# Kernel optimization log

Measured on AMD Instinct MI355X. Metric: run time of the kernel, lower is better.

## Reference

```python
import jax, jax.numpy as jnp
import numpy as np

EPS_BN = 1e-5


def _batchnorm(h, g, b):
    # training-mode BatchNorm1d over the flattened (B*N*k) axis
    mu = jnp.mean(h, axis=0)
    var = jnp.var(h, axis=0)
    return g * (h - mu) * jax.lax.rsqrt(var + EPS_BN) + b


def setup_inputs() -> dict:
    key = jax.random.key(0)
    ks = jax.random.split(key, 5)
    B, N = 4, 8192
    x = jax.random.normal(ks[0], (B, N, 3), dtype=jnp.float32)
    W1 = jax.random.normal(ks[1], (7, 10), dtype=jnp.float32) * (1.0 / np.sqrt(7.0))
    b1 = jax.random.normal(ks[2], (10,), dtype=jnp.float32) * 0.01
    W2 = jax.random.normal(ks[3], (10, 10), dtype=jnp.float32) * (1.0 / np.sqrt(10.0))
    b2 = jax.random.normal(ks[4], (10,), dtype=jnp.float32) * 0.01
    g1 = jnp.ones((10,), jnp.float32); be1 = jnp.zeros((10,), jnp.float32)
    g2 = jnp.ones((10,), jnp.float32); be2 = jnp.zeros((10,), jnp.float32)
    return {"x": x, "W1": W1, "b1": b1, "g1": g1, "be1": be1,
            "W2": W2, "b2": b2, "g2": g2, "be2": be2, "k": 9}


def reference(x, W1, b1, g1, be1, W2, b2, g2, be2, k):
    B, N, C = x.shape
    # --- kNN graph (brute force, self included as nearest) ---
    sq = jnp.sum(x * x, axis=-1)                                    # (B,N)
    d2 = sq[:, :, None] + sq[:, None, :] - 2.0 * jnp.einsum('bnc,bmc->bnm', x, x)
    _, idx = jax.lax.top_k(-d2, k + 1)                              # (B,N,k+1)
    nbrs = x[jnp.arange(B)[:, None, None], idx]                     # (B,N,k+1,3)
    rel = (nbrs - x[:, :, None, :])[:, :, 1:, :]                    # drop self -> (B,N,k,3)
    # --- sort neighbors by azimuth phi = atan2(y, x) ---
    phi = jnp.arctan2(rel[..., 1], rel[..., 0])                     # (B,N,k)
    order = jnp.argsort(phi, axis=-1)
    v1 = jnp.take_along_axis(rel, order[..., None], axis=2)         # (B,N,k,3)
    v2 = jnp.roll(v1, -1, axis=2)                                   # next neighbor (cyclic)
    # --- umbrella-style surface features ---
    centroids = 0.5 * (v1 + v2)
    normals = jnp.cross(v1, v2)
    normals = normals / (jnp.linalg.norm(normals, axis=-1, keepdims=True) + 1e-6)
    sign = jnp.where(normals[..., 0:1, 0] > 0, 1.0, -1.0)[..., None]  # (B,N,1,1)
    normals = normals * sign
    position = jnp.sum(normals * centroids, axis=-1, keepdims=True) / jnp.sqrt(jnp.asarray(3.0, x.dtype))
    feat = jnp.concatenate([centroids, normals, position], axis=-1)   # (B,N,k,7)
    feat = feat.reshape(B * N * k, 7)
    # --- tiny MLP + max-pool over k ---
    h = jax.nn.relu(_batchnorm(feat @ W1 + b1, g1, be1))
    h = jax.nn.relu(_batchnorm(h @ W2 + b2, g2, be2))
    return jnp.max(h.reshape(B, N, k, 10), axis=2)                  # (B,N,10)
```

## Files before the change

kernel.cpp:

```cpp
#include <hip/hip_runtime.h>
#include <math.h>
#include <float.h>
#include <stdint.h>

#define B_ 4
#define N_ 8192
#define K_ 9
#define NPTS (B_ * N_)
#define NROWS (NPTS * K_)
#define SPLIT 8
#define CHUNK (N_ / SPLIT)
#define NGROUP 32
#define GSIZE (CHUNK / NGROUP)
#define GSTRIDE 33
#define NCOPY 16

typedef float f4 __attribute__((ext_vector_type(4)));
typedef float f32x2 __attribute__((ext_vector_type(2)));

__device__ __forceinline__ f32x2 dist2_pk(f32x2 xx, f32x2 yy, f32x2 zz, f32x2 ww,
                                          f32x2 qx, f32x2 qy, f32x2 qz, f32x2 qw) {
  f32x2 t0 = qx * xx;
  f32x2 t1 = __builtin_elementwise_fma(qy, yy, t0);
  f32x2 t2 = __builtin_elementwise_fma(qz, zz, t1);
  f32x2 s  = qw + ww;
  f32x2 m2 = {-2.0f, -2.0f};
  return __builtin_elementwise_fma(t2, m2, s);
}

#define GDECL(G) float gd##G; int gi##G;
#define SCANG(G)                                                           \
  { float bgd = FLT_MAX; int bq = 0;                                       \
    _Pragma("clang loop unroll(disable)")                                  \
    for (int pr = 0; pr < 16; pr += 4) {                                   \
      const f4* cp = CH + (G * GSTRIDE + 2 * pr);                          \
      f4 A0 = cp[0], B0 = cp[1], A1 = cp[2], B1 = cp[3];                   \
      f4 A2 = cp[4], B2 = cp[5], A3 = cp[6], B3 = cp[7];                   \
      f32x2 dA = dist2_pk(__builtin_shufflevector(A0, A0, 0, 1),           \
                          __builtin_shufflevector(A0, A0, 2, 3),           \
                          __builtin_shufflevector(B0, B0, 0, 1),           \
                          __builtin_shufflevector(B0, B0, 2, 3),           \
                          qx2, qy2, qz2, qw2);                             \
      f32x2 dB = dist2_pk(__builtin_shufflevector(A1, A1, 0, 1),           \
                          __builtin_shufflevector(A1, A1, 2, 3),           \
                          __builtin_shufflevector(B1, B1, 0, 1),           \
                          __builtin_shufflevector(B1, B1, 2, 3),           \
                          qx2, qy2, qz2, qw2);                             \
      f32x2 dC = dist2_pk(__builtin_shufflevector(A2, A2, 0, 1),           \
                          __builtin_shufflevector(A2, A2, 2, 3),           \
                          __builtin_shufflevector(B2, B2, 0, 1),           \
                          __builtin_shufflevector(B2, B2, 2, 3),           \
                          qx2, qy2, qz2, qw2);                             \
      f32x2 dD = dist2_pk(__builtin_shufflevector(A3, A3, 0, 1),           \
                          __builtin_shufflevector(A3, A3, 2, 3),           \
                          __builtin_shufflevector(B3, B3, 0, 1),           \
                          __builtin_shufflevector(B3, B3, 2, 3),           \
                          qx2, qy2, qz2, qw2);                             \
      float d0 = dA.x, d1 = dA.y, d2 = dB.x, d3 = dB.y;                    \
      float d4 = dC.x, d5 = dC.y, d6 = dD.x, d7 = dD.y;                    \
      if (HS) {                                                            \
        int j = G * GSIZE + 2 * pr;                                        \
        d0 = (j + 0 == nl) ? FLT_MAX : d0;                                 \
        d1 = (j + 1 == nl) ? FLT_MAX : d1;                                 \
        d2 = (j + 2 == nl) ? FLT_MAX : d2;                                 \
        d3 = (j + 3 == nl) ? FLT_MAX : d3;                                 \
        d4 = (j + 4 == nl) ? FLT_MAX : d4;                                 \
        d5 = (j + 5 == nl) ? FLT_MAX : d5;                                 \
        d6 = (j + 6 == nl) ? FLT_MAX : d6;                                 \
        d7 = (j + 7 == nl) ? FLT_MAX : d7;                                 \
      }                                                                    \
      float m = fminf(fminf(fminf(d0, d1), fminf(d2, d3)),                 \
                      fminf(fminf(d4, d5), fminf(d6, d7)));                \
      bool lt = m < bgd; bgd = lt ? m : bgd; bq = lt ? pr : bq;            \
    }                                                                      \
    gd##G = bgd; gi##G = -1 - bq; }
#define LMC(G, S)                                                          \
  { bool lt = gd##G < wd##S;                                               \
    wd##S = lt ? gd##G : wd##S; wi##S = lt ? gi##G : wi##S;                \
    wg##S = lt ? G : wg##S; }
#define CMB(S)                                                             \
  { bool lt = wd##S < wda;                                                 \
    wda = lt ? wd##S : wda; wia = lt ? wi##S : wia; wga = lt ? wg##S : wga; }
#define WBK(G)                                                             \
  { bool m = (wg == G); gd##G = m ? nd : gd##G; gi##G = m ? ni : gi##G; }
#define TOURN8()                                                           \
  float e01d, e23d, e45d, e67d, f03d, f47d, md;                            \
  int   e01i, e23i, e45i, e67i, f03i, f47i, mi;                            \
  { bool t;                                                                \
    t = d1 < d0; e01d = t ? d1 : d0; e01i = t ? (j + 1) : (j + 0);         \
    t = d3 < d2; e23d = t ? d3 : d2; e23i = t ? (j + 3) : (j + 2);         \
    t = d5 < d4; e45d = t ? d5 : d4; e45i = t ? (j + 5) : (j + 4);         \
    t = d7 < d6; e67d = t ? d7 : d6; e67i = t ? (j + 7) : (j + 6);         \
    t = e23d < e01d; f03d = t ? e23d : e01d; f03i = t ? e23i : e01i;       \
    t = e67d < e45d; f47d = t ? e67d : e45d; f47i = t ? e67i : e45i;       \
    t = f47d < f03d; md = t ? f47d : f03d; mi = t ? f47i : f03i; }

template <bool HS>
__device__ __forceinline__ void knn_chunk(const f4* CH, f32x2 qx2, f32x2 qy2,
                                          f32x2 qz2, f32x2 qw2,
                                          int nl, int j0, int s, int p,
                                          uint2* __restrict__ PBDI) {
  GDECL(0) GDECL(1) GDECL(2) GDECL(3) GDECL(4) GDECL(5) GDECL(6) GDECL(7)
  GDECL(8) GDECL(9) GDECL(10) GDECL(11) GDECL(12) GDECL(13) GDECL(14) GDECL(15)
  GDECL(16) GDECL(17) GDECL(18) GDECL(19) GDECL(20) GDECL(21) GDECL(22) GDECL(23)
  GDECL(24) GDECL(25) GDECL(26) GDECL(27) GDECL(28) GDECL(29) GDECL(30) GDECL(31)

  SCANG(0) SCANG(1) SCANG(2) SCANG(3) SCANG(4) SCANG(5) SCANG(6) SCANG(7)
  SCANG(8) SCANG(9) SCANG(10) SCANG(11) SCANG(12) SCANG(13) SCANG(14) SCANG(15)
  SCANG(16) SCANG(17) SCANG(18) SCANG(19) SCANG(20) SCANG(21) SCANG(22) SCANG(23)
  SCANG(24) SCANG(25) SCANG(26) SCANG(27) SCANG(28) SCANG(29) SCANG(30) SCANG(31)

#pragma clang loop unroll(disable)
  for (int r = 0; r < K_; ++r) {
    float wda = gd0; int wia = gi0; int wga = 0;
    LMC(1,a) LMC(2,a) LMC(3,a) LMC(4,a) LMC(5,a) LMC(6,a) LMC(7,a)
    float wdb = gd8; int wib = gi8; int wgb = 8;
    LMC(9,b) LMC(10,b) LMC(11,b) LMC(12,b) LMC(13,b) LMC(14,b) LMC(15,b)
    float wdc = gd16; int wic = gi16; int wgc = 16;
    LMC(17,c) LMC(18,c) LMC(19,c) LMC(20,c) LMC(21,c) LMC(22,c) LMC(23,c)
    float wdd = gd24; int wid = gi24; int wgd = 24;
    LMC(25,d) LMC(26,d) LMC(27,d) LMC(28,d) LMC(29,d) LMC(30,d) LMC(31,d)
    CMB(b) CMB(c) CMB(d)
    float wd = wda; int wist = wia; int wg = wga;

    int ab = wg * GSTRIDE;
    int jb = wg * GSIZE;

    int wi;
    {
      int bq = (wist >= 0) ? 0 : (-1 - wist);
      const f4* cp = CH + (ab + 2 * bq);
      f4 A0 = cp[0], B0 = cp[1], A1 = cp[2], B1 = cp[3];
      f4 A2 = cp[4], B2 = cp[5], A3 = cp[6], B3 = cp[7];
      int j = jb + 2 * bq;
      f32x2 dA = dist2_pk(__builtin_shufflevector(A0, A0, 0, 1),
                          __builtin_shufflevector(A0, A0, 2, 3),
                          __builtin_shufflevector(B0, B0, 0, 1),
                          __builtin_shufflevector(B0, B0, 2, 3),
                          qx2, qy2, qz2, qw2);
      f32x2 dB = dist2_pk(__builtin_shufflevector(A1, A1, 0, 1),
                          __builtin_shufflevector(A1, A1, 2, 3),
                          __builtin_shufflevector(B1, B1, 0, 1),
                          __builtin_shufflevector(B1, B1, 2, 3),
                          qx2, qy2, qz2, qw2);
      f32x2 dC = dist2_pk(__builtin_shufflevector(A2, A2, 0, 1),
                          __builtin_shufflevector(A2, A2, 2, 3),
                          __builtin_shufflevector(B2, B2, 0, 1),
                          __builtin_shufflevector(B2, B2, 2, 3),
                          qx2, qy2, qz2, qw2);
      f32x2 dD = dist2_pk(__builtin_shufflevector(A3, A3, 0, 1),
                          __builtin_shufflevector(A3, A3, 2, 3),
                          __builtin_shufflevector(B3, B3, 0, 1),
                          __builtin_shufflevector(B3, B3, 2, 3),
                          qx2, qy2, qz2, qw2);
      float d0 = dA.x, d1 = dA.y, d2 = dB.x, d3 = dB.y;
      float d4 = dC.x, d5 = dC.y, d6 = dD.x, d7 = dD.y;
      if (HS) {
        d0 = (j + 0 == nl) ? FLT_MAX : d0;
        d1 = (j + 1 == nl) ? FLT_MAX : d1;
        d2 = (j + 2 == nl) ? FLT_MAX : d2;
        d3 = (j + 3 == nl) ? FLT_MAX : d3;
        d4 = (j + 4 == nl) ? FLT_MAX : d4;
        d5 = (j + 5 == nl) ? FLT_MAX : d5;
        d6 = (j + 6 == nl) ? FLT_MAX : d6;
        d7 = (j + 7 == nl) ? FLT_MAX : d7;
      }
      const int IMX = 0x7fffffff;
      int a0 = (d0 == wd) ? (j + 0) : IMX;
      int a1 = (d1 == wd) ? (j + 1) : IMX;
      int a2 = (d2 == wd) ? (j + 2) : IMX;
      int a3 = (d3 == wd) ? (j + 3) : IMX;
      int a4 = (d4 == wd) ? (j + 4) : IMX;
      int a5 = (d5 == wd) ? (j + 5) : IMX;
      int a6 = (d6 == wd) ? (j + 6) : IMX;
      int a7 = (d7 == wd) ? (j + 7) : IMX;
      int m01 = a0 < a1 ? a0 : a1;
      int m23 = a2 < a3 ? a2 : a3;
      int m45 = a4 < a5 ? a4 : a5;
      int m67 = a6 < a7 ? a6 : a7;
      int mA = m01 < m23 ? m01 : m23;
      int mB = m45 < m67 ? m45 : m67;
      int jm = mA < mB ? mA : mB;
      wi = (wist >= 0) ? wist : jm;
    }

    uint2 o; o.x = __float_as_uint(wd); o.y = (unsigned)(j0 + wi);
    PBDI[(size_t)(s * K_ + r) * NPTS + p] = o;

    float nd = FLT_MAX; int ni = 0;
#pragma clang loop unroll(disable)
    for (int pr = 0; pr < 16; pr += 4) {
      const f4* cp = CH + (ab + 2 * pr);
      f4 A0 = cp[0], B0 = cp[1], A1 = cp[2], B1 = cp[3];
      f4 A2 = cp[4], B2 = cp[5], A3 = cp[6], B3 = cp[7];
      int j = jb + 2 * pr;
      f32x2 dA = dist2_pk(__builtin_shufflevector(A0, A0, 0, 1),
                          __builtin_shufflevector(A0, A0, 2, 3),
                          __builtin_shufflevector(B0, B0, 0, 1),
                          __builtin_shufflevector(B0, B0, 2, 3),
                          qx2, qy2, qz2, qw2);
      f32x2 dB = dist2_pk(__builtin_shufflevector(A1, A1, 0, 1),
                          __builtin_shufflevector(A1, A1, 2, 3),
                          __builtin_shufflevector(B1, B1, 0, 1),
                          __builtin_shufflevector(B1, B1, 2, 3),
                          qx2, qy2, qz2, qw2);
      f32x2 dC = dist2_pk(__builtin_shufflevector(A2, A2, 0, 1),
                          __builtin_shufflevector(A2, A2, 2, 3),
                          __builtin_shufflevector(B2, B2, 0, 1),
                          __builtin_shufflevector(B2, B2, 2, 3),
                          qx2, qy2, qz2, qw2);
      f32x2 dD = dist2_pk(__builtin_shufflevector(A3, A3, 0, 1),
                          __builtin_shufflevector(A3, A3, 2, 3),
                          __builtin_shufflevector(B3, B3, 0, 1),
                          __builtin_shufflevector(B3, B3, 2, 3),
                          qx2, qy2, qz2, qw2);
      float d0 = dA.x, d1 = dA.y, d2 = dB.x, d3 = dB.y;
      float d4 = dC.x, d5 = dC.y, d6 = dD.x, d7 = dD.y;
      if (HS) {
        d0 = (j + 0 == nl) ? FLT_MAX : d0;
        d1 = (j + 1 == nl) ? FLT_MAX : d1;
        d2 = (j + 2 == nl) ? FLT_MAX : d2;
        d3 = (j + 3 == nl) ? FLT_MAX : d3;
        d4 = (j + 4 == nl) ? FLT_MAX : d4;
        d5 = (j + 5 == nl) ? FLT_MAX : d5;
        d6 = (j + 6 == nl) ? FLT_MAX : d6;
        d7 = (j + 7 == nl) ? FLT_MAX : d7;
      }
      bool k0 = (d0 > wd) | ((d0 == wd) & ((j + 0) > wi));
      bool k1 = (d1 > wd) | ((d1 == wd) & ((j + 1) > wi));
      bool k2 = (d2 > wd) | ((d2 == wd) & ((j + 2) > wi));
      bool k3 = (d3 > wd) | ((d3 == wd) & ((j + 3) > wi));
      bool k4 = (d4 > wd) | ((d4 == wd) & ((j + 4) > wi));
      bool k5 = (d5 > wd) | ((d5 == wd) & ((j + 5) > wi));
      bool k6 = (d6 > wd) | ((d6 == wd) & ((j + 6) > wi));
      bool k7 = (d7 > wd) | ((d7 == wd) & ((j + 7) > wi));
      d0 = k0 ? d0 : FLT_MAX;
      d1 = k1 ? d1 : FLT_MAX;
      d2 = k2 ? d2 : FLT_MAX;
      d3 = k3 ? d3 : FLT_MAX;
      d4 = k4 ? d4 : FLT_MAX;
      d5 = k5 ? d5 : FLT_MAX;
      d6 = k6 ? d6 : FLT_MAX;
      d7 = k7 ? d7 : FLT_MAX;
      TOURN8();
      bool lt = md < nd; nd = lt ? md : nd; ni = lt ? mi : ni;
    }
    WBK(0) WBK(1) WBK(2) WBK(3) WBK(4) WBK(5) WBK(6) WBK(7)
    WBK(8) WBK(9) WBK(10) WBK(11) WBK(12) WBK(13) WBK(14) WBK(15)
    WBK(16) WBK(17) WBK(18) WBK(19) WBK(20) WBK(21) WBK(22) WBK(23)
    WBK(24) WBK(25) WBK(26) WBK(27) WBK(28) WBK(29) WBK(30) WBK(31)
  }
}

__launch_bounds__(128, 4)
__global__ void k_knn(const float* __restrict__ x, uint2* __restrict__ PBDI,
                      double* __restrict__ ACC) {
  __shared__ f4 CH[NGROUP * GSTRIDE];
  int bid = blockIdx.x;
  if (bid == 0) {
    for (int t = threadIdx.x; t < NCOPY * 40; t += 128) ACC[t] = 0.0;
  }
  int pg = bid >> 3;
  int s = bid & (SPLIT - 1);
  int p = pg * 128 + threadIdx.x;
  int b = p >> 13;
  int n = p & (N_ - 1);
  int bO = b * N_;
  int j0 = s * CHUNK;

  const float* xq = x + 3 * (size_t)p;
  float qa = xq[0], qb = xq[1], qc = xq[2];
  float qw = qa * qa + qb * qb + qc * qc;
  f32x2 qx2 = {qa, qa}, qy2 = {qb, qb}, qz2 = {qc, qc}, qw2 = {qw, qw};

  for (int u = threadIdx.x; u < CHUNK / 2; u += 128) {
    const float* xp = x + 3 * (size_t)(bO + j0 + 2 * u);
    float a0 = xp[0], b0 = xp[1], c0 = xp[2];
    float a1 = xp[3], b1 = xp[4], c1 = xp[5];
    int G = u >> 4, rr = u & 15;
    f4 lo = {a0, a1, b0, b1};
    f4 hi = {c0, c1, a0 * a0 + b0 * b0 + c0 * c0, a1 * a1 + b1 * b1 + c1 * c1};
    CH[G * GSTRIDE + 2 * rr] = lo;
    CH[G * GSTRIDE + 2 * rr + 1] = hi;
  }
  __syncthreads();

  int n0 = (pg * 128) & (N_ - 1);
  int nl = n - j0;
  if (s == (n0 >> 10)) knn_chunk<true >(CH, qx2, qy2, qz2, qw2, nl, j0, s, p, PBDI);
  else                 knn_chunk<false>(CH, qx2, qy2, qz2, qw2, nl, j0, s, p, PBDI);
}

#define LVL(bdv, biv)                                                     \
  { bool lt = cd < (bdv); float td = (bdv); int ti = (biv);               \
    (bdv) = lt ? cd : (bdv); (biv) = lt ? ci : (biv);                     \
    cd = lt ? td : cd; ci = lt ? ti : ci; }
#define INS9ALL()                                                         \
  LVL(b0d, b0i) LVL(b1d, b1i) LVL(b2d, b2i) LVL(b3d, b3i) LVL(b4d, b4i)  \
  LVL(b5d, b5i) LVL(b6d, b6i) LVL(b7d, b7i) LVL(b8d, b8i)
#define TOP9_DECL()                                                       \
  float b0d = FLT_MAX, b1d = FLT_MAX, b2d = FLT_MAX, b3d = FLT_MAX,       \
        b4d = FLT_MAX, b5d = FLT_MAX, b6d = FLT_MAX, b7d = FLT_MAX,       \
        b8d = FLT_MAX;                                                    \
  int b0i = 0, b1i = 0, b2i = 0, b3i = 0, b4i = 0, b5i = 0, b6i = 0,      \
      b7i = 0, b8i = 0;

#define MKREL(T)                                                          \
  float rx##T, ry##T, rz##T, ph##T;                                       \
  { const float* mp = x + 3 * (size_t)(bO + b##T##i);                     \
    rx##T = mp[0] - qa; ry##T = mp[1] - qb; rz##T = mp[2] - qc;           \
    ph##T = atan2f(ry##T, rx##T); }

#define CE(A, Bv)                                                         \
  { bool lt = ph##Bv < ph##A; float t0;                                   \
    t0 = ph##A; ph##A = lt ? ph##Bv : t0; ph##Bv = lt ? t0 : ph##Bv;      \
    t0 = rx##A; rx##A = lt ? rx##Bv : t0; rx##Bv = lt ? t0 : rx##Bv;      \
    t0 = ry##A; ry##A = lt ? ry##Bv : t0; ry##Bv = lt ? t0 : ry##Bv;      \
    t0 = rz##A; rz##A = lt ? rz##Bv : t0; rz##Bv = lt ? t0 : rz##Bv; }

#define ST9(arr, v0, v1, v2, v3, v4, v5, v6, v7, v8)                      \
  arr[0 * 64 + pl] = v0; arr[1 * 64 + pl] = v1; arr[2 * 64 + pl] = v2;    \
  arr[3 * 64 + pl] = v3; arr[4 * 64 + pl] = v4; arr[5 * 64 + pl] = v5;    \
  arr[6 * 64 + pl] = v6; arr[7 * 64 + pl] = v7; arr[8 * 64 + pl] = v8;

__launch_bounds__(256, 4)
__global__ void k_tail1(const float* __restrict__ x, const uint2* __restrict__ PBDI,
                        const float* __restrict__ W1, const float* __restrict__ b1,
                        float* __restrict__ H1, double* __restrict__ ACC) {
  __shared__ float  LMD[64 * 37];
  __shared__ int    LMI[64 * 37];
  __shared__ float  LREL[3][9 * 64];
  __shared__ float  LSGN[64];
  __shared__ double sred[4][20];

  int q = threadIdx.x >> 6;
  int pl = threadIdx.x & 63;
  int pbase = blockIdx.x * 64;
  int p = pbase + pl;

  {
    TOP9_DECL();
#pragma clang loop unroll_count(2)
    for (int e = 0; e < 2 * K_; ++e) {
      uint2 v = PBDI[(size_t)(q * 2 * K_ + e) * NPTS + p];
      float cd = __uint_as_float(v.x);
      int ci = (int)v.y;
      INS9ALL();
    }
    int base = pl * 37 + q * 9;
    LMD[base + 0] = b0d; LMD[base + 1] = b1d; LMD[base + 2] = b2d;
    LMD[base + 3] = b3d; LMD[base + 4] = b4d; LMD[base + 5] = b5d;
    LMD[base + 6] = b6d; LMD[base + 7] = b7d; LMD[base + 8] = b8d;
    LMI[base + 0] = b0i; LMI[base + 1] = b1i; LMI[base + 2] = b2i;
    LMI[base + 3] = b3i; LMI[base + 4] = b4i; LMI[base + 5] = b5i;
    LMI[base + 6] = b6i; LMI[base + 7] = b7i; LMI[base + 8] = b8i;
  }
  __syncthreads();

  if (q == 0) {
    int b = p >> 13;
    int bO = b * N_;
    const float* xq = x + 3 * (size_t)p;
    float qa = xq[0], qb = xq[1], qc = xq[2];

    TOP9_DECL();
#pragma clang loop unroll_count(3)
    for (int e = 0; e < 4 * K_; ++e) {
      float cd = LMD[pl * 37 + e];
      int ci = LMI[pl * 37 + e];
      INS9ALL();
    }

    MKREL(0) MKREL(1) MKREL(2) MKREL(3) MKREL(4)
    MKREL(5) MKREL(6) MKREL(7) MKREL(8)

    CE(0,1)
    CE(1,2) CE(0,1)
    CE(2,3) CE(1,2) CE(0,1)
    CE(3,4) CE(2,3) CE(1,2) CE(0,1)
    CE(4,5) CE(3,4) CE(2,3) CE(1,2) CE(0,1)
    CE(5,6) CE(4,5) CE(3,4) CE(2,3) CE(1,2) CE(0,1)
    CE(6,7) CE(5,6) CE(4,5) CE(3,4) CE(2,3) CE(1,2) CE(0,1)
    CE(7,8) CE(6,7) CE(5,6) CE(4,5) CE(3,4) CE(2,3) CE(1,2) CE(0,1)

    float nx0 = ry0 * rz1 - rz0 * ry1;
    float ny0 = rz0 * rx1 - rx0 * rz1;
    float nz0 = rx0 * ry1 - ry0 * rx1;
    float nrm0 = sqrtf(nx0 * nx0 + ny0 * ny0 + nz0 * nz0) + 1e-6f;
    LSGN[pl] = ((nx0 / nrm0) > 0.0f) ? 1.0f : -1.0f;

    ST9(LREL[0], rx0, rx1, rx2, rx3, rx4, rx5, rx6, rx7, rx8)
    ST9(LREL[1], ry0, ry1, ry2, ry3, ry4, ry5, ry6, ry7, ry8)
    ST9(LREL[2], rz0, rz1, rz2, rz3, rz4, rz5, rz6, rz7, rz8)
  }
  __syncthreads();

  double sum[10], ss[10];
#pragma unroll
  for (int c = 0; c < 10; ++c) { sum[c] = 0.0; ss[c] = 0.0; }

#pragma clang loop unroll(disable)
  for (int rl = threadIdx.x; rl < 9 * 64; rl += 256) {
    int t = rl >> 6;
    int pp = rl & 63;
    int t2 = (t + 1 == K_) ? 0 : t + 1;
    float v1x = LREL[0][t * 64 + pp];
    float v1y = LREL[1][t * 64 + pp];
    float v1z = LREL[2][t * 64 + pp];
    float v2x = LREL[0][t2 * 64 + pp];
    float v2y = LREL[1][t2 * 64 + pp];
    float v2z = LREL[2][t2 * 64 + pp];
    float sgn = LSGN[pp];

    float cx = 0.5f * (v1x + v2x);
    float cy = 0.5f * (v1y + v2y);
    float cz = 0.5f * (v1z + v2z);
    float nx = v1y * v2z - v1z * v2y;
    float ny = v1z * v2x - v1x * v2z;
    float nz = v1x * v2y - v1y * v2x;
    float nrm = sqrtf(nx * nx + ny * ny + nz * nz) + 1e-6f;
    nx /= nrm; ny /= nrm; nz /= nrm;
    nx *= sgn; ny *= sgn; nz *= sgn;
    float pos = (nx * cx + ny * cy + nz * cz) / 1.7320508075688772f;

    float fv[7] = {cx, cy, cz, nx, ny, nz, pos};
#pragma unroll
    for (int c = 0; c < 10; ++c) {
      float h = b1[c];
#pragma unroll
      for (int rr = 0; rr < 7; ++rr) h = fmaf(fv[rr], W1[rr * 10 + c], h);
      H1[(size_t)c * NROWS + (size_t)t * NPTS + pbase + pp] = h;
      double hd = (double)h;
      sum[c] += hd; ss[c] += hd * hd;
    }
  }

  int lane = threadIdx.x & 63, wv = threadIdx.x >> 6;
#pragma unroll
  for (int c = 0; c < 10; ++c) {
    double a = sum[c];
#pragma unroll
    for (int off = 32; off > 0; off >>= 1) a += __shfl_down(a, off);
    if (lane == 0) sred[wv][c] = a;
    double qq = ss[c];
#pragma unroll
    for (int off = 32; off > 0; off >>= 1) qq += __shfl_down(qq, off);
    if (lane == 0) sred[wv][10 + c] = qq;
  }
  __syncthreads();
  if (threadIdx.x < 20) {
    atomicAdd(&ACC[(blockIdx.x & (NCOPY - 1)) * 40 + threadIdx.x],
              sred[0][threadIdx.x] + sred[1][threadIdx.x] +
              sred[2][threadIdx.x] + sred[3][threadIdx.x]);
  }
}

__launch_bounds__(64)
__global__ void k_mlp2(const float* __restrict__ H1, double* __restrict__ ACC,
                       const float* __restrict__ g1, const float* __restrict__ be1,
                       const float* __restrict__ W2, const float* __restrict__ b2,
                       const float* __restrict__ g2, float* __restrict__ EXT) {
  __shared__ float MR[20];
  __shared__ double sred[20];
  if (threadIdx.x < 20) {
    int c = threadIdx.x % 10;
    int half = threadIdx.x / 10;
    double s0 = 0.0, s1 = 0.0;
#pragma unroll
    for (int cc = 0; cc < NCOPY; ++cc) {
      s0 += ACC[cc * 40 + c];
      s1 += ACC[cc * 40 + 10 + c];
    }
    double mu = s0 / (double)NROWS;
    double var = s1 / (double)NROWS - mu * mu;
    MR[threadIdx.x] = half ? (float)(1.0 / sqrt(var + 1e-5)) : (float)mu;
  }
  __syncthreads();

  int p = blockIdx.x * 64 + threadIdx.x;
  double sum[10], ss[10];
  float ext[10], sg[10];
#pragma unroll
  for (int c = 0; c < 10; ++c) {
    sum[c] = 0.0; ss[c] = 0.0;
    sg[c] = g2[c];
    ext[c] = (sg[c] >= 0.0f) ? -FLT_MAX : FLT_MAX;
  }

#pragma clang loop unroll(disable)
  for (int t = 0; t < K_; ++t) {
    float v[10];
#pragma unroll
    for (int c = 0; c < 10; ++c) {
      float h = H1[(size_t)c * NROWS + (size_t)t * NPTS + p];
      float z = g1[c] * (h - MR[c]) * MR[10 + c] + be1[c];
      v[c] = z > 0.0f ? z : 0.0f;
    }
#pragma unroll
    for (int c = 0; c < 10; ++c) {
      float h = b2[c];
#pragma unroll
      for (int u = 0; u < 10; ++u) h = fmaf(v[u], W2[u * 10 + c], h);
      sum[c] += (double)h;
      ss[c] += (double)h * (double)h;
      ext[c] = (sg[c] >= 0.0f) ? fmaxf(ext[c], h) : fminf(ext[c], h);
    }
  }

#pragma unroll
  for (int c = 0; c < 10; ++c)
    EXT[(size_t)c * NPTS + p] = ext[c];

#pragma unroll
  for (int c = 0; c < 10; ++c) {
    double a = sum[c];
#pragma unroll
    for (int off = 32; off > 0; off >>= 1) a += __shfl_down(a, off);
    if (threadIdx.x == 0) sred[c] = a;
    double qq = ss[c];
#pragma unroll
    for (int off = 32; off > 0; off >>= 1) qq += __shfl_down(qq, off);
    if (threadIdx.x == 0) sred[10 + c] = qq;
  }
  __syncthreads();
  if (threadIdx.x < 20) {
    atomicAdd(&ACC[(blockIdx.x & (NCOPY - 1)) * 40 + 20 + threadIdx.x],
              sred[threadIdx.x]);
  }
}

__launch_bounds__(64)
__global__ void k_out(const float* __restrict__ EXT, const double* __restrict__ ACC,
                      const float* __restrict__ g2, const float* __restrict__ be2,
                      float* __restrict__ out) {
  __shared__ float MR[20];
  if (threadIdx.x < 20) {
    int c = threadIdx.x % 10;
    int half = threadIdx.x / 10;
    double s0 = 0.0, s1 = 0.0;
#pragma unroll
    for (int cc = 0; cc < NCOPY; ++cc) {
      s0 += ACC[cc * 40 + 20 + c];
      s1 += ACC[cc * 40 + 30 + c];
    }
    double mu = s0 / (double)NROWS;
    double var = s1 / (double)NROWS - mu * mu;
    MR[threadIdx.x] = half ? (float)(1.0 / sqrt(var + 1e-5)) : (float)mu;
  }
  __syncthreads();

  int p = blockIdx.x * 64 + threadIdx.x;
#pragma unroll
  for (int c = 0; c < 10; ++c) {
    float h = EXT[(size_t)c * NPTS + p];
    float z = g2[c] * (h - MR[c]) * MR[10 + c] + be2[c];
    z = z > 0.0f ? z : 0.0f;
    out[(size_t)p * 10 + c] = z;
  }
}

extern "C" void kernel_launch(void* const* d_in, const int* in_sizes, int n_in,
                              void* d_out, int out_size, void* d_ws, size_t ws_size,
                              hipStream_t stream) {
  (void)in_sizes; (void)n_in; (void)out_size; (void)ws_size;
  const float* x  = (const float*)d_in[0];
  const float* W1 = (const float*)d_in[1];
  const float* b1 = (const float*)d_in[2];
  const float* g1 = (const float*)d_in[3];
  const float* be1= (const float*)d_in[4];
  const float* W2 = (const float*)d_in[5];
  const float* b2 = (const float*)d_in[6];
  const float* g2 = (const float*)d_in[7];
  const float* be2= (const float*)d_in[8];
  float* out = (float*)d_out;

  char* base = (char*)d_ws;
  uint2*  PBDI = (uint2*)base;
  float*  H1 = (float*)(base + (size_t)SPLIT * K_ * NPTS * 8);
  double* ACC = (double*)(H1 + (size_t)10 * NROWS);
  float*  EXT = (float*)PBDI;

  k_knn<<<(NPTS / 128) * SPLIT, 128, 0, stream>>>(x, PBDI, ACC);
  k_tail1<<<NPTS / 64, 256, 0, stream>>>(x, PBDI, W1, b1, H1, ACC);
  k_mlp2<<<NPTS / 64, 64, 0, stream>>>(H1, ACC, g1, be1, W2, b2, g2, EXT);
  k_out<<<NPTS / 64, 64, 0, stream>>>(EXT, ACC, g2, be2, out);
}
```

Before: 215.7 us.

## Parallelize k_mlp2 across neighbors with one wave per k slot

k_mlp2 previously looped over the 9 neighbors serially within a 64-thread block. Now each block has 576 threads, one wavefront per neighbor slot. Each wave computes the second-layer outputs in parallel, stores them in LDS, and then reduces max/min over k from shared memory. The intent is more parallelism and latency hiding for this small kernel. The cost is more LDS use, a block-wide barrier, and more shuffle reductions per row.

```diff
diff --git a/kernel.cpp b/kernel.cpp
--- a/kernel.cpp
+++ b/kernel.cpp
@@ -455,16 +455,18 @@
   }
 }
 
-__launch_bounds__(64)
+__launch_bounds__(576)
 __global__ void k_mlp2(const float* __restrict__ H1, double* __restrict__ ACC,
                        const float* __restrict__ g1, const float* __restrict__ be1,
                        const float* __restrict__ W2, const float* __restrict__ b2,
                        const float* __restrict__ g2, float* __restrict__ EXT) {
   __shared__ float MR[20];
-  __shared__ double sred[20];
-  if (threadIdx.x < 20) {
-    int c = threadIdx.x % 10;
-    int half = threadIdx.x / 10;
+  __shared__ float H2L[10][K_][64];
+  __shared__ double sred[9][20];
+  int tid = threadIdx.x;
+  if (tid < 20) {
+    int c = tid % 10;
+    int half = tid / 10;
     double s0 = 0.0, s1 = 0.0;
 #pragma unroll
     for (int cc = 0; cc < NCOPY; ++cc) {
@@ -473,59 +475,66 @@
     }
     double mu = s0 / (double)NROWS;
     double var = s1 / (double)NROWS - mu * mu;
-    MR[threadIdx.x] = half ? (float)(1.0 / sqrt(var + 1e-5)) : (float)mu;
-  }
-  __syncthreads();
-
-  int p = blockIdx.x * 64 + threadIdx.x;
-  double sum[10], ss[10];
-  float ext[10], sg[10];
+    MR[tid] = half ? (float)(1.0 / sqrt(var + 1e-5)) : (float)mu;
+  }
+  __syncthreads();
+
+  int t = tid >> 6;
+  int pl = tid & 63;
+  int pbase = blockIdx.x * 64;
+  int p = pbase + pl;
+
+  float v[10];
 #pragma unroll
   for (int c = 0; c < 10; ++c) {
-    sum[c] = 0.0; ss[c] = 0.0;
-    sg[c] = g2[c];
-    ext[c] = (sg[c] >= 0.0f) ? -FLT_MAX : FLT_MAX;
-  }
-
-#pragma clang loop unroll(disable)
-  for (int t = 0; t < K_; ++t) {
-    float v[10];
-#pragma unroll
-    for (int c = 0; c < 10; ++c) {
-      float h = H1[(size_t)c * NROWS + (size_t)t * NPTS + p];
-      float z = g1[c] * (h - MR[c]) * MR[10 + c] + be1[c];
-      v[c] = z > 0.0f ? z : 0.0f;
-    }
-#pragma unroll
-    for (int c = 0; c < 10; ++c) {
-      float h = b2[c];
-#pragma unroll
-      for (int u = 0; u < 10; ++u) h = fmaf(v[u], W2[u * 10 + c], h);
-      sum[c] += (double)h;
-      ss[c] += (double)h * (double)h;
-      ext[c] = (sg[c] >= 0.0f) ? fmaxf(ext[c], h) : fminf(ext[c], h);
-    }
-  }
-
-#pragma unroll
-  for (int c = 0; c < 10; ++c)
-    EXT[(size_t)c * NPTS + p] = ext[c];
-
+    float h = H1[(size_t)c * NROWS + (size_t)t * NPTS + p];
+    float z = g1[c] * (h - MR[c]) * MR[10 + c] + be1[c];
+    v[c] = z > 0.0f ? z : 0.0f;
+  }
+
+  float h2v[10];
 #pragma unroll
   for (int c = 0; c < 10; ++c) {
-    double a = sum[c];
+    float h = b2[c];
+#pragma unroll
+    for (int u = 0; u < 10; ++u) h = fmaf(v[u], W2[u * 10 + c], h);
+    h2v[c] = h;
+    H2L[c][t][pl] = h;
+  }
+
+  int wv = tid >> 6;
+#pragma unroll
+  for (int c = 0; c < 10; ++c) {
+    double a = (double)h2v[c];
 #pragma unroll
     for (int off = 32; off > 0; off >>= 1) a += __shfl_down(a, off);
-    if (threadIdx.x == 0) sred[c] = a;
-    double qq = ss[c];
+    if (pl == 0) sred[wv][c] = a;
+    double qq = (double)h2v[c] * (double)h2v[c];
 #pragma unroll
     for (int off = 32; off > 0; off >>= 1) qq += __shfl_down(qq, off);
-    if (threadIdx.x == 0) sred[10 + c] = qq;
-  }
-  __syncthreads();
-  if (threadIdx.x < 20) {
-    atomicAdd(&ACC[(blockIdx.x & (NCOPY - 1)) * 40 + 20 + threadIdx.x],
-              sred[threadIdx.x]);
+    if (pl == 0) sred[wv][10 + c] = qq;
+  }
+  __syncthreads();
+  if (tid < 20) {
+    double a = 0.0;
+#pragma unroll
+    for (int w = 0; w < 9; ++w) a += sred[w][tid];
+    atomicAdd(&ACC[(blockIdx.x & (NCOPY - 1)) * 40 + 20 + tid], a);
+  }
+
+  for (int task = tid; task < 640; task += 576) {
+    int c = task >> 6;
+    int pp = task & 63;
+    float sgc = g2[c];
+    float e = H2L[c][0][pp];
+    if (sgc >= 0.0f) {
+#pragma unroll
+      for (int u = 1; u < K_; ++u) e = fmaxf(e, H2L[c][u][pp]);
+    } else {
+#pragma unroll
+      for (int u = 1; u < K_; ++u) e = fminf(e, H2L[c][u][pp]);
+    }
+    EXT[(size_t)c * NPTS + pbase + pp] = e;
   }
 }
 
@@ -582,6 +591,6 @@
 
   k_knn<<<(NPTS / 128) * SPLIT, 128, 0, stream>>>(x, PBDI, ACC);
   k_tail1<<<NPTS / 64, 256, 0, stream>>>(x, PBDI, W1, b1, H1, ACC);
-  k_mlp2<<<NPTS / 64, 64, 0, stream>>>(H1, ACC, g1, be1, W2, b2, g2, EXT);
+  k_mlp2<<<NPTS / 64, 576, 0, stream>>>(H1, ACC, g1, be1, W2, b2, g2, EXT);
   k_out<<<NPTS / 64, 64, 0, stream>>>(EXT, ACC, g2, be2, out);
 }
```

Result: no change. 215.4 us (-0.1%).
